# Performance work log

Measured on AMD Instinct MI355X. Metric: run time of the kernel, lower is better.

## Reference

```python
import jax, jax.numpy as jnp
import numpy as np

POOLED_H = 7
POOLED_W = 7
SPATIAL_SCALE = 0.0625
B, C, H, W = 8, 256, 48, 48
R = 300
IMG = 768  # = H / SPATIAL_SCALE


def setup_inputs() -> dict:
    key = jax.random.key(0)
    k1, k2, k3, k4 = jax.random.split(key, 4)
    features = jax.random.normal(k1, (B, C, H, W), dtype=jnp.float32)
    # rois: (batch_idx, x1, y1, x2, y2) in input-image coords
    bidx = jax.random.randint(k2, (R, 1), 0, B).astype(jnp.float32)
    tl = jax.random.uniform(k3, (R, 2), minval=0.0, maxval=IMG - 64.0)
    wh = jax.random.uniform(k4, (R, 2), minval=32.0, maxval=320.0)
    br = jnp.minimum(tl + wh, IMG - 1.0)
    rois = jnp.concatenate([bidx, tl, br], axis=1).astype(jnp.float32)
    return {"features": features, "rois": rois}


def _hat_integral(x, grid):
    """Integral from -inf to x of the unit hat basis function centered at each
    grid point g (support [g-1, g+1], peak 1, total mass 1).
    x: [..., 1-broadcastable], grid: [G] -> returns [..., G]."""
    t = x[..., None] - (grid - 1.0)
    return jnp.where(
        t <= 0.0, 0.0,
        jnp.where(t <= 1.0, 0.5 * t * t,
                  jnp.where(t <= 2.0, 1.0 - 0.5 * (2.0 - t) ** 2, 1.0)))


def reference(features, rois):
    # Precise RoI Pooling: exact double integral of the bilinear interpolant
    # over each bin, divided by bin area. Bilinear interp (with zero padding
    # outside the map, as in the CUDA PrRoIPoolingGetData) is
    #   f(u,v) = sum_{j,i} feat[j,i] * hat_j(v) * hat_i(u)
    # so the bin integral factorizes into per-axis hat-integral weights.
    Bf, Cf, Hf, Wf = features.shape
    bidx = rois[:, 0].astype(jnp.int32)
    x1 = rois[:, 1] * SPATIAL_SCALE
    y1 = rois[:, 2] * SPATIAL_SCALE
    x2 = rois[:, 3] * SPATIAL_SCALE
    y2 = rois[:, 4] * SPATIAL_SCALE
    roi_w = jnp.maximum(x2 - x1, 0.0)
    roi_h = jnp.maximum(y2 - y1, 0.0)
    bin_w = roi_w / POOLED_W  # [R]
    bin_h = roi_h / POOLED_H

    ph = jnp.arange(POOLED_H, dtype=jnp.float32)
    pw = jnp.arange(POOLED_W, dtype=jnp.float32)
    ya = y1[:, None] + ph[None, :] * bin_h[:, None]  # [R, PH]
    yb = ya + bin_h[:, None]
    xa = x1[:, None] + pw[None, :] * bin_w[:, None]  # [R, PW]
    xb = xa + bin_w[:, None]

    gy = jnp.arange(Hf, dtype=jnp.float32)
    gx = jnp.arange(Wf, dtype=jnp.float32)
    Wy = _hat_integral(yb, gy) - _hat_integral(ya, gy)  # [R, PH, H]
    Wx = _hat_integral(xb, gx) - _hat_integral(xa, gx)  # [R, PW, W]

    feat = features[bidx]  # [R, C, H, W]
    t = jnp.einsum('rpj,rcji->rcpi', Wy, feat)   # integrate over y
    num = jnp.einsum('rqi,rcpi->rcpq', Wx, t)    # integrate over x -> [R,C,PH,PW]

    area = (bin_w * bin_h)[:, None, None, None]  # win_size per ROI
    out = jnp.where(area > 0.0, num / jnp.where(area > 0.0, area, 1.0), 0.0)
    return out
```

## Files before the change

### kernel.cpp

```cpp
#include <hip/hip_runtime.h>


#define PH 7
#define PW 7
#define NBINS 49
#define SCALE 0.0625f
#define CH 256
#define FH 48
#define FW 48
#define RNUM 300
#define CB 8
#define QN 2
#define MAXJ 23
#define ROWF 28

__device__ __forceinline__ float hat_int(float x, float g) {
    float t = x - (g - 1.0f);
    if (t <= 0.0f) return 0.0f;
    if (t <= 1.0f) return 0.5f * t * t;
    if (t <= 2.0f) { float u = 2.0f - t; return 1.0f - 0.5f * u * u; }
    return 1.0f;
}

__global__ __launch_bounds__(256)
void prroi_fused(const float* __restrict__ feat,
                 const float* __restrict__ rois,
                 float* __restrict__ out) {
    const int cblk = blockIdx.x;
    const int r    = blockIdx.y;
    const int c0   = cblk * CB;
    const int tid  = threadIdx.x;

    __shared__ float patch[MAXJ * ROWF * CB];
    __shared__ float rs[PW * MAXJ * CB];
    __shared__ float s_wy[PH][6];
    __shared__ float s_wx[PW][6];
    __shared__ int   s_bj[PH];
    __shared__ int   s_bi[PW];

    const float* roi = rois + r * 5;
    const int   b  = (int)roi[0];
    const float x1 = roi[1] * SCALE, y1 = roi[2] * SCALE;
    const float x2 = roi[3] * SCALE, y2 = roi[4] * SCALE;
    const float roi_w = fmaxf(x2 - x1, 0.0f), roi_h = fmaxf(y2 - y1, 0.0f);
    const float bin_w = roi_w / (float)PW, bin_h = roi_h / (float)PH;
    const float area = bin_w * bin_h;
    const float inv_area = (area > 0.0f) ? (1.0f / area) : 0.0f;

    const float ylo = fminf(y1, y2), yhi = fmaxf(y1, y2);
    const float xlo = fminf(x1, x2), xhi = fmaxf(x1, x2);
    const int j1 = min(FH - 1, (int)floorf(yhi) + 1);
    const int i1 = min(FW - 1, (int)floorf(xhi) + 1);
    const int J0 = min(max(0, (int)floorf(ylo) - 1), FH - 6);
    const int I0 = min(max(0, (int)floorf(xlo) - 1) & ~3, FW - 8);
    const int JROWS = min(FH - J0, max(j1 - J0 + 1, 6));
    int NI4 = min(((i1 - I0) >> 2) + 1, (FW - I0) >> 2);
    NI4 = max(NI4, 2);

    if (tid < PH + PW) {
        if (tid < PH) {
            const int ph = tid;
            const float ya = y1 + ph * bin_h, yb = ya + bin_h;
            const int base = min(max((int)floorf(ya) - 1, J0), J0 + JROWS - 6);
            s_bj[ph] = base - J0;
#pragma unroll
            for (int k = 0; k < 6; ++k) {
                const float g = (float)(base + k);
                s_wy[ph][k] = hat_int(yb, g) - hat_int(ya, g);
            }
        } else {
            const int pw = tid - PH;
            const float xa = x1 + pw * bin_w, xb = xa + bin_w;
            const int base = min(max((int)floorf(xa) - 1, I0), I0 + 4 * NI4 - 6);
            s_bi[pw] = base - I0;
#pragma unroll
            for (int k = 0; k < 6; ++k) {
                const float g = (float)(base + k);
                s_wx[pw][k] = hat_int(xb, g) - hat_int(xa, g);
            }
        }
    }

    const float* fb = feat + (size_t)(b * CH + c0) * FH * FW;
    for (int u = tid; u < QN * MAXJ * 7; u += 256) {
        const int q   = u / (MAXJ * 7);
        const int rem = u - q * (MAXJ * 7);
        const int j   = rem / 7;
        const int i4  = rem - j * 7;
        if (j < JROWS && i4 < NI4) {
            const int ig = I0 + 4 * i4;
            const float* src = fb + ((size_t)(4 * q) * FH + (J0 + j)) * FW + ig;
            const float4 v0 = *(const float4*)(src);
            const float4 v1 = *(const float4*)(src + FH * FW);
            const float4 v2 = *(const float4*)(src + 2 * FH * FW);
            const float4 v3 = *(const float4*)(src + 3 * FH * FW);
            float* dst = &patch[((size_t)j * ROWF + 4 * i4) * CB + 4 * q];
            *(float4*)(dst + 0 * CB) = make_float4(v0.x, v1.x, v2.x, v3.x);
            *(float4*)(dst + 1 * CB) = make_float4(v0.y, v1.y, v2.y, v3.y);
            *(float4*)(dst + 2 * CB) = make_float4(v0.z, v1.z, v2.z, v3.z);
            *(float4*)(dst + 3 * CB) = make_float4(v0.w, v1.w, v2.w, v3.w);
        }
    }
    __syncthreads();

    for (int u = tid; u < JROWS * 14; u += 256) {
        const int j   = u / 14;
        const int rem = u - j * 14;
        const int pw  = rem >> 1;
        const int q   = rem & 1;
        const int bi  = s_bi[pw];
        const float* base = &patch[((size_t)j * ROWF + bi) * CB + 4 * q];
        float ax = 0.0f, ay = 0.0f, az = 0.0f, aw = 0.0f;
#pragma unroll
        for (int ii = 0; ii < 6; ++ii) {
            const float w = s_wx[pw][ii];
            const float4 v = *(const float4*)(base + ii * CB);
            ax += w * v.x; ay += w * v.y; az += w * v.z; aw += w * v.w;
        }
        *(float4*)(&rs[((size_t)pw * MAXJ + j) * CB + 4 * q]) =
            make_float4(ax, ay, az, aw);
    }
    __syncthreads();

    const int bin = tid & 63;
    const int cp  = tid >> 6;
    if (bin < NBINS) {
        const int ph = bin / PW;
        const int pw = bin - ph * PW;
        const int bj = s_bj[ph];
        const float* rbase = &rs[((size_t)pw * MAXJ + bj) * CB + 2 * cp];
        float ax = 0.0f, ay = 0.0f;
#pragma unroll
        for (int jj = 0; jj < 6; ++jj) {
            const float w = s_wy[ph][jj];
            const float2 v = *(const float2*)(rbase + jj * CB);
            ax += w * v.x; ay += w * v.y;
        }
        float* o = out + ((size_t)r * CH + c0 + 2 * cp) * NBINS + bin;
        o[0]     = ax * inv_area;
        o[NBINS] = ay * inv_area;
    }
}

extern "C" void kernel_launch(void* const* d_in, const int* in_sizes, int n_in,
                              void* d_out, int out_size, void* d_ws, size_t ws_size,
                              hipStream_t stream) {
    const float* feat = (const float*)d_in[0];
    const float* rois = (const float*)d_in[1];
    float* out = (float*)d_out;

    prroi_fused<<<dim3(CH / CB, RNUM), 256, 0, stream>>>(feat, rois, out);
}
```

Baseline: 91.79 us.

## Precompute per-ROI weights in a separate prep kernel and load into registers

Splits the fused kernel into a small prep kernel that computes per-ROI hat-integral weights, base offsets and patch bounds into a workspace buffer, and a main kernel that reads them. The main kernel now loads its weights into registers before the feature staging and unrolls the x-integration loop into two fixed slots, instead of computing weights redundantly in each of 32 channel blocks and sharing them via shared memory. This removes repeated per-block ROI math and shared-memory weight reads, at the cost of an extra launch and global reads of the parameter block.

```diff
diff --git a/kernel.cpp b/kernel.cpp
--- a/kernel.cpp
+++ b/kernel.cpp
@@ -13,6 +13,7 @@
 #define QN 2
 #define MAXJ 23
 #define ROWF 28
+#define PRM 112
 
 __device__ __forceinline__ float hat_int(float x, float g) {
     float t = x - (g - 1.0f);
@@ -23,20 +24,10 @@
 }
 
 __global__ __launch_bounds__(256)
-void prroi_fused(const float* __restrict__ feat,
-                 const float* __restrict__ rois,
-                 float* __restrict__ out) {
-    const int cblk = blockIdx.x;
-    const int r    = blockIdx.y;
-    const int c0   = cblk * CB;
-    const int tid  = threadIdx.x;
-
-    __shared__ float patch[MAXJ * ROWF * CB];
-    __shared__ float rs[PW * MAXJ * CB];
-    __shared__ float s_wy[PH][6];
-    __shared__ float s_wx[PW][6];
-    __shared__ int   s_bj[PH];
-    __shared__ int   s_bi[PW];
+void prroi_prep(const float* __restrict__ rois, float* __restrict__ prm) {
+    const int r = blockIdx.x * 4 + (threadIdx.x >> 6);
+    const int t = threadIdx.x & 63;
+    if (r >= RNUM || t >= 15) return;
 
     const float* roi = rois + r * 5;
     const int   b  = (int)roi[0];
@@ -57,28 +48,83 @@
     int NI4 = min(((i1 - I0) >> 2) + 1, (FW - I0) >> 2);
     NI4 = max(NI4, 2);
 
-    if (tid < PH + PW) {
-        if (tid < PH) {
-            const int ph = tid;
-            const float ya = y1 + ph * bin_h, yb = ya + bin_h;
-            const int base = min(max((int)floorf(ya) - 1, J0), J0 + JROWS - 6);
-            s_bj[ph] = base - J0;
-#pragma unroll
-            for (int k = 0; k < 6; ++k) {
-                const float g = (float)(base + k);
-                s_wy[ph][k] = hat_int(yb, g) - hat_int(ya, g);
-            }
-        } else {
-            const int pw = tid - PH;
-            const float xa = x1 + pw * bin_w, xb = xa + bin_w;
-            const int base = min(max((int)floorf(xa) - 1, I0), I0 + 4 * NI4 - 6);
-            s_bi[pw] = base - I0;
-#pragma unroll
-            for (int k = 0; k < 6; ++k) {
-                const float g = (float)(base + k);
-                s_wx[pw][k] = hat_int(xb, g) - hat_int(xa, g);
-            }
-        }
+    float* p = prm + (size_t)r * PRM;
+    if (t < PH) {
+        const int ph = t;
+        const float ya = y1 + ph * bin_h, yb = ya + bin_h;
+        const int base = min(max((int)floorf(ya) - 1, J0), J0 + JROWS - 6);
+        p[84 + ph] = __int_as_float(base - J0);
+#pragma unroll
+        for (int k = 0; k < 6; ++k) {
+            const float g = (float)(base + k);
+            p[ph * 6 + k] = hat_int(yb, g) - hat_int(ya, g);
+        }
+    } else if (t < PH + PW) {
+        const int pw = t - PH;
+        const float xa = x1 + pw * bin_w, xb = xa + bin_w;
+        const int base = min(max((int)floorf(xa) - 1, I0), I0 + 4 * NI4 - 6);
+        p[91 + pw] = __int_as_float(base - I0);
+#pragma unroll
+        for (int k = 0; k < 6; ++k) {
+            const float g = (float)(base + k);
+            p[42 + pw * 6 + k] = hat_int(xb, g) - hat_int(xa, g);
+        }
+    } else {
+        p[98]  = inv_area;
+        p[99]  = __int_as_float(b);
+        p[100] = __int_as_float(J0);
+        p[101] = __int_as_float(I0);
+        p[102] = __int_as_float(JROWS);
+        p[103] = __int_as_float(NI4);
+    }
+}
+
+__global__ __launch_bounds__(256)
+void prroi_main(const float* __restrict__ feat,
+                const float* __restrict__ prm,
+                float* __restrict__ out) {
+    const int cblk = blockIdx.x;
+    const int r    = blockIdx.y;
+    const int c0   = cblk * CB;
+    const int tid  = threadIdx.x;
+
+    __shared__ float patch[MAXJ * ROWF * CB];
+    __shared__ float rs[PW * MAXJ * CB];
+
+    const float* p = prm + (size_t)r * PRM;
+    const int b     = __float_as_int(p[99]);
+    const int J0    = __float_as_int(p[100]);
+    const int I0    = __float_as_int(p[101]);
+    const int JROWS = __float_as_int(p[102]);
+    const int NI4   = __float_as_int(p[103]);
+
+    const int nA = JROWS * 14;
+    const int v1 = tid, v2 = tid + 256;
+    int pw1 = 0, q1 = 0, j1r = 0, pw2 = 0, q2 = 0, j2r = 0, bi1 = 0, bi2 = 0;
+    float wxa[6], wxb[6];
+    const bool a1 = v1 < nA, a2 = v2 < nA;
+    if (a1) {
+        j1r = v1 / 14; const int rem = v1 - j1r * 14; pw1 = rem >> 1; q1 = rem & 1;
+        bi1 = __float_as_int(p[91 + pw1]);
+#pragma unroll
+        for (int k = 0; k < 6; ++k) wxa[k] = p[42 + pw1 * 6 + k];
+    }
+    if (a2) {
+        j2r = v2 / 14; const int rem = v2 - j2r * 14; pw2 = rem >> 1; q2 = rem & 1;
+        bi2 = __float_as_int(p[91 + pw2]);
+#pragma unroll
+        for (int k = 0; k < 6; ++k) wxb[k] = p[42 + pw2 * 6 + k];
+    }
+
+    const int bin = tid & 63;
+    const int cp  = tid >> 6;
+    float wy[6]; int bj = 0, phv = 0, pwv = 0;
+    float inv_area = p[98];
+    if (bin < NBINS) {
+        phv = bin / PW; pwv = bin - phv * PW;
+        bj = __float_as_int(p[84 + phv]);
+#pragma unroll
+        for (int k = 0; k < 6; ++k) wy[k] = p[phv * 6 + k];
     }
 
     const float* fb = feat + (size_t)(b * CH + c0) * FH * FW;
@@ -91,48 +137,50 @@
             const int ig = I0 + 4 * i4;
             const float* src = fb + ((size_t)(4 * q) * FH + (J0 + j)) * FW + ig;
             const float4 v0 = *(const float4*)(src);
-            const float4 v1 = *(const float4*)(src + FH * FW);
-            const float4 v2 = *(const float4*)(src + 2 * FH * FW);
-            const float4 v3 = *(const float4*)(src + 3 * FH * FW);
+            const float4 v1v = *(const float4*)(src + FH * FW);
+            const float4 v2v = *(const float4*)(src + 2 * FH * FW);
+            const float4 v3v = *(const float4*)(src + 3 * FH * FW);
             float* dst = &patch[((size_t)j * ROWF + 4 * i4) * CB + 4 * q];
-            *(float4*)(dst + 0 * CB) = make_float4(v0.x, v1.x, v2.x, v3.x);
-            *(float4*)(dst + 1 * CB) = make_float4(v0.y, v1.y, v2.y, v3.y);
-            *(float4*)(dst + 2 * CB) = make_float4(v0.z, v1.z, v2.z, v3.z);
-            *(float4*)(dst + 3 * CB) = make_float4(v0.w, v1.w, v2.w, v3.w);
+            *(float4*)(dst + 0 * CB) = make_float4(v0.x, v1v.x, v2v.x, v3v.x);
+            *(float4*)(dst + 1 * CB) = make_float4(v0.y, v1v.y, v2v.y, v3v.y);
+            *(float4*)(dst + 2 * CB) = make_float4(v0.z, v1v.z, v2v.z, v3v.z);
+            *(float4*)(dst + 3 * CB) = make_float4(v0.w, v1v.w, v2v.w, v3v.w);
         }
     }
     __syncthreads();
 
-    for (int u = tid; u < JROWS * 14; u += 256) {
-        const int j   = u / 14;
-        const int rem = u - j * 14;
-        const int pw  = rem >> 1;
-        const int q   = rem & 1;
-        const int bi  = s_bi[pw];
-        const float* base = &patch[((size_t)j * ROWF + bi) * CB + 4 * q];
+    if (a1) {
+        const float* base = &patch[((size_t)j1r * ROWF + bi1) * CB + 4 * q1];
         float ax = 0.0f, ay = 0.0f, az = 0.0f, aw = 0.0f;
 #pragma unroll
         for (int ii = 0; ii < 6; ++ii) {
-            const float w = s_wx[pw][ii];
+            const float w = wxa[ii];
             const float4 v = *(const float4*)(base + ii * CB);
             ax += w * v.x; ay += w * v.y; az += w * v.z; aw += w * v.w;
         }
-        *(float4*)(&rs[((size_t)pw * MAXJ + j) * CB + 4 * q]) =
+        *(float4*)(&rs[((size_t)pw1 * MAXJ + j1r) * CB + 4 * q1]) =
             make_float4(ax, ay, az, aw);
     }
+    if (a2) {
+        const float* base = &patch[((size_t)j2r * ROWF + bi2) * CB + 4 * q2];
+        float ax = 0.0f, ay = 0.0f, az = 0.0f, aw = 0.0f;
+#pragma unroll
+        for (int ii = 0; ii < 6; ++ii) {
+            const float w = wxb[ii];
+            const float4 v = *(const float4*)(base + ii * CB);
+            ax += w * v.x; ay += w * v.y; az += w * v.z; aw += w * v.w;
+        }
+        *(float4*)(&rs[((size_t)pw2 * MAXJ + j2r) * CB + 4 * q2]) =
+            make_float4(ax, ay, az, aw);
+    }
     __syncthreads();
 
-    const int bin = tid & 63;
-    const int cp  = tid >> 6;
     if (bin < NBINS) {
-        const int ph = bin / PW;
-        const int pw = bin - ph * PW;
-        const int bj = s_bj[ph];
-        const float* rbase = &rs[((size_t)pw * MAXJ + bj) * CB + 2 * cp];
+        const float* rbase = &rs[((size_t)pwv * MAXJ + bj) * CB + 2 * cp];
         float ax = 0.0f, ay = 0.0f;
 #pragma unroll
         for (int jj = 0; jj < 6; ++jj) {
-            const float w = s_wy[ph][jj];
+            const float w = wy[jj];
             const float2 v = *(const float2*)(rbase + jj * CB);
             ax += w * v.x; ay += w * v.y;
         }
@@ -148,6 +196,8 @@
     const float* feat = (const float*)d_in[0];
     const float* rois = (const float*)d_in[1];
     float* out = (float*)d_out;
-
-    prroi_fused<<<dim3(CH / CB, RNUM), 256, 0, stream>>>(feat, rois, out);
-}
+    float* prm = (float*)d_ws;
+
+    prroi_prep<<<(RNUM + 3) / 4, 256, 0, stream>>>(rois, prm);
+    prroi_main<<<dim3(CH / CB, RNUM), 256, 0, stream>>>(feat, prm, out);
+}
```

After: 87.79 us. 4.4% less time.

## Precompute per-ROI weights in a prep kernel and register-load them in main

Applied to the files above, without the earlier changes.

Per-ROI hat-integral weights, base offsets and patch bounds move into a small prep kernel that writes a 128-float parameter block per ROI to workspace. Before, each of the 32 channel blocks per ROI recomputed them. The main kernel loads its weights straight into registers with float4 reads, folds inv_area into the y weights, and restructures the patch-load and x-pass loops with fixed per-thread mappings and fully unrolled FMAs. This removes redundant per-block weight computation, the shared-memory weight arrays and their sync, at the cost of a second kernel launch and a global round trip for the parameters.

```diff
diff --git a/kernel.cpp b/kernel.cpp
--- a/kernel.cpp
+++ b/kernel.cpp
@@ -10,9 +10,9 @@
 #define FW 48
 #define RNUM 300
 #define CB 8
-#define QN 2
 #define MAXJ 23
 #define ROWF 28
+#define PRM 128
 
 __device__ __forceinline__ float hat_int(float x, float g) {
     float t = x - (g - 1.0f);
@@ -23,20 +23,10 @@
 }
 
 __global__ __launch_bounds__(256)
-void prroi_fused(const float* __restrict__ feat,
-                 const float* __restrict__ rois,
-                 float* __restrict__ out) {
-    const int cblk = blockIdx.x;
-    const int r    = blockIdx.y;
-    const int c0   = cblk * CB;
-    const int tid  = threadIdx.x;
-
-    __shared__ float patch[MAXJ * ROWF * CB];
-    __shared__ float rs[PW * MAXJ * CB];
-    __shared__ float s_wy[PH][6];
-    __shared__ float s_wx[PW][6];
-    __shared__ int   s_bj[PH];
-    __shared__ int   s_bi[PW];
+void prroi_prep(const float* __restrict__ rois, float* __restrict__ prm) {
+    const int r = blockIdx.x * 4 + (threadIdx.x >> 6);
+    const int t = threadIdx.x & 63;
+    if (r >= RNUM || t >= 15) return;
 
     const float* roi = rois + r * 5;
     const int   b  = (int)roi[0];
@@ -57,88 +47,161 @@
     int NI4 = min(((i1 - I0) >> 2) + 1, (FW - I0) >> 2);
     NI4 = max(NI4, 2);
 
-    if (tid < PH + PW) {
-        if (tid < PH) {
-            const int ph = tid;
-            const float ya = y1 + ph * bin_h, yb = ya + bin_h;
-            const int base = min(max((int)floorf(ya) - 1, J0), J0 + JROWS - 6);
-            s_bj[ph] = base - J0;
+    float* p = prm + (size_t)r * PRM;
+    if (t < PH) {
+        const int ph = t;
+        const float ya = y1 + ph * bin_h, yb = ya + bin_h;
+        const int base = min(max((int)floorf(ya) - 1, J0), J0 + JROWS - 6);
 #pragma unroll
-            for (int k = 0; k < 6; ++k) {
-                const float g = (float)(base + k);
-                s_wy[ph][k] = hat_int(yb, g) - hat_int(ya, g);
-            }
-        } else {
-            const int pw = tid - PH;
-            const float xa = x1 + pw * bin_w, xb = xa + bin_w;
-            const int base = min(max((int)floorf(xa) - 1, I0), I0 + 4 * NI4 - 6);
-            s_bi[pw] = base - I0;
+        for (int k = 0; k < 6; ++k) {
+            const float g = (float)(base + k);
+            p[ph * 8 + k] = (hat_int(yb, g) - hat_int(ya, g)) * inv_area;
+        }
+        p[ph * 8 + 6] = __int_as_float(base - J0);
+        p[ph * 8 + 7] = 0.0f;
+    } else if (t < PH + PW) {
+        const int pw = t - PH;
+        const float xa = x1 + pw * bin_w, xb = xa + bin_w;
+        const int base = min(max((int)floorf(xa) - 1, I0), I0 + 4 * NI4 - 6);
 #pragma unroll
-            for (int k = 0; k < 6; ++k) {
-                const float g = (float)(base + k);
-                s_wx[pw][k] = hat_int(xb, g) - hat_int(xa, g);
-            }
-        }
-    }
-
-    const float* fb = feat + (size_t)(b * CH + c0) * FH * FW;
-    for (int u = tid; u < QN * MAXJ * 7; u += 256) {
-        const int q   = u / (MAXJ * 7);
-        const int rem = u - q * (MAXJ * 7);
-        const int j   = rem / 7;
-        const int i4  = rem - j * 7;
-        if (j < JROWS && i4 < NI4) {
-            const int ig = I0 + 4 * i4;
-            const float* src = fb + ((size_t)(4 * q) * FH + (J0 + j)) * FW + ig;
+        for (int k = 0; k < 6; ++k) {
+            const float g = (float)(base + k);
+            p[56 + pw * 8 + k] = hat_int(xb, g) - hat_int(xa, g);
+        }
+        p[56 + pw * 8 + 6] = __int_as_float(base - I0);
+        p[56 + pw * 8 + 7] = 0.0f;
+    } else {
+        p[112] = __int_as_float(b);
+        p[113] = __int_as_float(J0);
+        p[114] = __int_as_float(I0);
+        p[115] = __int_as_float(JROWS | (NI4 << 8));
+    }
+}
+
+__global__ __launch_bounds__(256)
+void prroi_main(const float* __restrict__ feat,
+                const float* __restrict__ prm,
+                float* __restrict__ out) {
+    const int cblk = blockIdx.x;
+    const int r    = blockIdx.y;
+    const int c0   = cblk * CB;
+    const int tid  = threadIdx.x;
+
+    __shared__ float patch[MAXJ * ROWF * CB];
+    __shared__ float rs[PW * MAXJ * CB];
+
+    const float* p = prm + (size_t)r * PRM;
+
+    const float4 misc = *(const float4*)(p + 112);
+    const int qA  = tid & 1;
+    const int pwA = (tid >> 1) & 7;
+    const int jA  = tid >> 4;
+    const float4 wxv0 = *(const float4*)(p + 56 + pwA * 8);
+    const float4 wxv1 = *(const float4*)(p + 56 + pwA * 8 + 4);
+    const int bin = tid & 63;
+    const int cp  = tid >> 6;
+    const int phv = bin / 7;
+    const int pwv = bin - phv * 7;
+    const float4 wyv0 = *(const float4*)(p + phv * 8);
+    const float4 wyv1 = *(const float4*)(p + phv * 8 + 4);
+
+    const int b      = __float_as_int(misc.x);
+    const int J0     = __float_as_int(misc.y);
+    const int I0     = __float_as_int(misc.z);
+    const int packed = __float_as_int(misc.w);
+    const int JROWS  = packed & 255;
+    const int NI4    = packed >> 8;
+    const int biA    = __float_as_int(wxv1.z);
+    const int bj     = __float_as_int(wyv1.z);
+
+    const int i4P = tid & 7;
+    const int qP  = (tid >> 3) & 1;
+    const int jbP = tid >> 4;
+    if (i4P < NI4) {
+        const float* src = feat + (size_t)(b * CH + c0 + 4 * qP) * FH * FW
+                         + (size_t)(J0 + jbP) * FW + I0 + 4 * i4P;
+        float* dst = &patch[((size_t)jbP * ROWF + 4 * i4P) * CB + 4 * qP];
+        for (int j = jbP; j < JROWS; j += 16) {
             const float4 v0 = *(const float4*)(src);
             const float4 v1 = *(const float4*)(src + FH * FW);
             const float4 v2 = *(const float4*)(src + 2 * FH * FW);
             const float4 v3 = *(const float4*)(src + 3 * FH * FW);
-            float* dst = &patch[((size_t)j * ROWF + 4 * i4) * CB + 4 * q];
             *(float4*)(dst + 0 * CB) = make_float4(v0.x, v1.x, v2.x, v3.x);
             *(float4*)(dst + 1 * CB) = make_float4(v0.y, v1.y, v2.y, v3.y);
             *(float4*)(dst + 2 * CB) = make_float4(v0.z, v1.z, v2.z, v3.z);
             *(float4*)(dst + 3 * CB) = make_float4(v0.w, v1.w, v2.w, v3.w);
+            src += 16 * FW;
+            dst += 16 * ROWF * CB;
         }
     }
     __syncthreads();
 
-    for (int u = tid; u < JROWS * 14; u += 256) {
-        const int j   = u / 14;
-        const int rem = u - j * 14;
-        const int pw  = rem >> 1;
-        const int q   = rem & 1;
-        const int bi  = s_bi[pw];
-        const float* base = &patch[((size_t)j * ROWF + bi) * CB + 4 * q];
-        float ax = 0.0f, ay = 0.0f, az = 0.0f, aw = 0.0f;
-#pragma unroll
-        for (int ii = 0; ii < 6; ++ii) {
-            const float w = s_wx[pw][ii];
-            const float4 v = *(const float4*)(base + ii * CB);
-            ax += w * v.x; ay += w * v.y; az += w * v.z; aw += w * v.w;
-        }
-        *(float4*)(&rs[((size_t)pw * MAXJ + j) * CB + 4 * q]) =
-            make_float4(ax, ay, az, aw);
+    if (pwA < PW) {
+        const float* base0 = &patch[((size_t)jA * ROWF + biA) * CB + 4 * qA];
+        float* rdst = &rs[((size_t)pwA * MAXJ + jA) * CB + 4 * qA];
+        for (int j = jA; j < JROWS; j += 16) {
+            float ax, ay, az, aw;
+            {
+                const float4 v = *(const float4*)(base0 + 0 * CB);
+                ax = wxv0.x * v.x; ay = wxv0.x * v.y; az = wxv0.x * v.z; aw = wxv0.x * v.w;
+            }
+            {
+                const float4 v = *(const float4*)(base0 + 1 * CB);
+                ax += wxv0.y * v.x; ay += wxv0.y * v.y; az += wxv0.y * v.z; aw += wxv0.y * v.w;
+            }
+            {
+                const float4 v = *(const float4*)(base0 + 2 * CB);
+                ax += wxv0.z * v.x; ay += wxv0.z * v.y; az += wxv0.z * v.z; aw += wxv0.z * v.w;
+            }
+            {
+                const float4 v = *(const float4*)(base0 + 3 * CB);
+                ax += wxv0.w * v.x; ay += wxv0.w * v.y; az += wxv0.w * v.z; aw += wxv0.w * v.w;
+            }
+            {
+                const float4 v = *(const float4*)(base0 + 4 * CB);
+                ax += wxv1.x * v.x; ay += wxv1.x * v.y; az += wxv1.x * v.z; aw += wxv1.x * v.w;
+            }
+            {
+                const float4 v = *(const float4*)(base0 + 5 * CB);
+                ax += wxv1.y * v.x; ay += wxv1.y * v.y; az += wxv1.y * v.z; aw += wxv1.y * v.w;
+            }
+            *(float4*)rdst = make_float4(ax, ay, az, aw);
+            base0 += 16 * ROWF * CB;
+            rdst  += 16 * CB;
+        }
     }
     __syncthreads();
 
-    const int bin = tid & 63;
-    const int cp  = tid >> 6;
     if (bin < NBINS) {
-        const int ph = bin / PW;
-        const int pw = bin - ph * PW;
-        const int bj = s_bj[ph];
-        const float* rbase = &rs[((size_t)pw * MAXJ + bj) * CB + 2 * cp];
+        const float* rbase = &rs[((size_t)pwv * MAXJ + bj) * CB + 2 * cp];
         float ax = 0.0f, ay = 0.0f;
-#pragma unroll
-        for (int jj = 0; jj < 6; ++jj) {
-            const float w = s_wy[ph][jj];
-            const float2 v = *(const float2*)(rbase + jj * CB);
-            ax += w * v.x; ay += w * v.y;
+        {
+            const float2 v = *(const float2*)(rbase + 0 * CB);
+            ax += wyv0.x * v.x; ay += wyv0.x * v.y;
+        }
+        {
+            const float2 v = *(const float2*)(rbase + 1 * CB);
+            ax += wyv0.y * v.x; ay += wyv0.y * v.y;
+        }
+        {
+            const float2 v = *(const float2*)(rbase + 2 * CB);
+            ax += wyv0.z * v.x; ay += wyv0.z * v.y;
+        }
+        {
+            const float2 v = *(const float2*)(rbase + 3 * CB);
+            ax += wyv0.w * v.x; ay += wyv0.w * v.y;
+        }
+        {
+            const float2 v = *(const float2*)(rbase + 4 * CB);
+            ax += wyv1.x * v.x; ay += wyv1.x * v.y;
+        }
+        {
+            const float2 v = *(const float2*)(rbase + 5 * CB);
+            ax += wyv1.y * v.x; ay += wyv1.y * v.y;
         }
         float* o = out + ((size_t)r * CH + c0 + 2 * cp) * NBINS + bin;
-        o[0]     = ax * inv_area;
-        o[NBINS] = ay * inv_area;
+        o[0]     = ax;
+        o[NBINS] = ay;
     }
 }
 
@@ -148,6 +211,8 @@
     const float* feat = (const float*)d_in[0];
     const float* rois = (const float*)d_in[1];
     float* out = (float*)d_out;
-
-    prroi_fused<<<dim3(CH / CB, RNUM), 256, 0, stream>>>(feat, rois, out);
-}
+    float* prm = (float*)d_ws;
+
+    prroi_prep<<<(RNUM + 3) / 4, 256, 0, stream>>>(rois, prm);
+    prroi_main<<<dim3(CH / CB, RNUM), 256, 0, stream>>>(feat, prm, out);
+}
```

Result: faster. 89.28 us (-2.7%).
